# Kernel optimization log

Hardware: AMD Instinct MI355X
Metric: run time of the kernel (lower is better)

The kernel has to match this reference:

```python
import jax, jax.numpy as jnp
import numpy as np

T, D, H, E, K = 4096, 2048, 1408, 8, 2  # tokens, d_model, d_intermediate, n_experts, top_k


def setup_inputs() -> dict:
    key = jax.random.key(0)
    ks = jax.random.split(key, 5)
    x = jax.random.normal(ks[0], (T, D), dtype=jnp.float32)
    # distinct top-k expert ids per token (router output)
    indices = jnp.argsort(jax.random.uniform(ks[1], (T, E)), axis=-1)[:, :K].astype(jnp.int32)
    w = jax.random.uniform(ks[2], (T, K), dtype=jnp.float32) + 0.1
    weights = w / jnp.sum(w, axis=-1, keepdims=True)
    # stacked expert params: fc1 [E, 2H, D], fc2 [E, D, H] (nn.Linear layout)
    w1 = jax.random.normal(ks[3], (E, 2 * H, D), dtype=jnp.float32) * (D ** -0.5)
    w2 = jax.random.normal(ks[4], (E, D, H), dtype=jnp.float32) * (H ** -0.5)
    return {"x": x, "weights": weights, "indices": indices, "w1": w1, "w2": w2}


def reference(x, weights, indices, w1, w2):
    # combine weight per (expert, token): sum of routing weights where token routed to expert e
    onehot = jax.nn.one_hot(indices, E, dtype=x.dtype)          # [T, K, E]
    cw = jnp.einsum('tk,tke->et', weights, onehot)              # [E, T]

    def body(y, inp):
        w1_i, w2_i, cw_i = inp
        h = x @ w1_i.T                                          # [T, 2H]
        u, g = jnp.split(h, 2, axis=-1)                         # value, gate (chunk order of GatedMLP)
        out = (u * jax.nn.silu(g)) @ w2_i.T                     # [T, D]
        return y + out * cw_i[:, None], None

    y, _ = jax.lax.scan(body, jnp.zeros_like(x), (w1, w2, cw))
    return y
```

## Files before the change

### kernel.cpp

```cpp
#include <hip/hip_runtime.h>
#include <stdint.h>

#define T_TOK 4096
#define DMODEL 2048
#define HDIM 1408
#define NEXP 8
#define TOPK 2

#define BM 256
#define BN 256
#define BK 32
#define MAX_TILES (T_TOK * TOPK / BM + NEXP)
#define SMEM_BYTES (131072 + 1024)

typedef unsigned short u16;
typedef __bf16 bf16x8 __attribute__((ext_vector_type(8)));
typedef float f32x4 __attribute__((ext_vector_type(4)));

__device__ __forceinline__ u16 f2bf(float f) {
  union { float f; uint32_t u; } v; v.f = f;
  uint32_t r = (v.u + 0x7FFFu + ((v.u >> 16) & 1u)) >> 16;
  return (u16)r;
}

__device__ __forceinline__ void gll16(const void* g, void* l) {
  __builtin_amdgcn_global_load_lds(
      (__attribute__((address_space(1))) void*)(uintptr_t)g,
      (__attribute__((address_space(3))) void*)l, 16, 0, 0);
}

__global__ __launch_bounds__(256) void convert_all(
    const float* __restrict__ x, const float* __restrict__ w1,
    const float* __restrict__ w2, u16* __restrict__ xb,
    u16* __restrict__ w1b, u16* __restrict__ w2b) {
  const long c0 = (long)T_TOK * DMODEL / 8;
  const long c1 = (long)NEXP * 2 * HDIM * DMODEL / 8;
  const long c2 = (long)NEXP * DMODEL * HDIM / 8;
  const long total = c0 + c1 + c2;
  const long stride = (long)gridDim.x * blockDim.x;
  for (long i = blockIdx.x * (long)blockDim.x + threadIdx.x; i < total; i += stride) {
    const float* s; u16* d; long j;
    if (i < c0)            { s = x;  d = xb;  j = i; }
    else if (i < c0 + c1)  { s = w1; d = w1b; j = i - c0; }
    else                   { s = w2; d = w2b; j = i - c0 - c1; }
    const float4* sp = (const float4*)s + j * 2;
    float4 v0 = sp[0], v1 = sp[1];
    union { u16 us[8]; uint4 u4; } o;
    o.us[0] = f2bf(v0.x); o.us[1] = f2bf(v0.y); o.us[2] = f2bf(v0.z); o.us[3] = f2bf(v0.w);
    o.us[4] = f2bf(v1.x); o.us[5] = f2bf(v1.y); o.us[6] = f2bf(v1.z); o.us[7] = f2bf(v1.w);
    *((uint4*)(d + j * 8)) = o.u4;
  }
}

__global__ void route_kernel(const int* __restrict__ idx, int* __restrict__ cnt,
                             int* __restrict__ perm) {
  int i = blockIdx.x * blockDim.x + threadIdx.x;
  if (i < T_TOK * TOPK) {
    int e = idx[i];
    int p = atomicAdd(&cnt[e], 1);
    perm[e * T_TOK + p] = i;
  }
}

__global__ void tilemap_kernel(const int* __restrict__ cnt, int* __restrict__ tmap,
                               int* __restrict__ ntp) {
  if (threadIdx.x == 0 && blockIdx.x == 0) {
    int nt = 0;
    for (int e = 0; e < NEXP; ++e) {
      int n = cnt[e];
      for (int r = 0; r < n; r += BM) tmap[nt++] = (e << 16) | r;
    }
    *ntp = nt;
  }
}


template <int H, int VMN>
__device__ __forceinline__ void phase_core(const char* bc, const int (&aoffR)[8],
                                           const int (&boffR)[4], f32x4 (&acc)[8][4]) {
  bf16x8 a_[4], b_[4];
#pragma unroll
  for (int m = 0; m < 4; ++m) a_[m] = *(const bf16x8*)(bc + aoffR[H * 4 + m]);
#pragma unroll
  for (int n = 0; n < 4; ++n) b_[n] = *(const bf16x8*)(bc + boffR[n]);
  if constexpr (VMN == 8) {
    asm volatile("s_waitcnt vmcnt(8)" ::: "memory");
    __builtin_amdgcn_sched_barrier(0);
  } else if constexpr (VMN == 4) {
    asm volatile("s_waitcnt vmcnt(4)" ::: "memory");
    __builtin_amdgcn_sched_barrier(0);
  } else if constexpr (VMN == 0) {
    asm volatile("s_waitcnt vmcnt(0)" ::: "memory");
    __builtin_amdgcn_sched_barrier(0);
  }
  __builtin_amdgcn_s_barrier();
  __builtin_amdgcn_s_setprio(1);
#pragma unroll
  for (int m = 0; m < 4; ++m)
#pragma unroll
    for (int n = 0; n < 4; ++n)
      acc[H * 4 + m][n] = __builtin_amdgcn_mfma_f32_16x16x32_bf16(
          a_[m], b_[n], acc[H * 4 + m][n], 0, 0, 0);
  __builtin_amdgcn_s_setprio(0);
  __builtin_amdgcn_s_barrier();
}

template <int MODE>
__global__ __launch_bounds__(512, 2) void moe_gemm(
    const u16* __restrict__ A, const u16* __restrict__ Bw,
    const float* __restrict__ wts, const int* __restrict__ perm,
    const int* __restrict__ cnt, const int* __restrict__ tmap,
    const int* __restrict__ ntp, u16* __restrict__ act,
    float* __restrict__ pairs) {
  constexpr int KD = (MODE == 0) ? DMODEL : HDIM;
  constexpr int NT = KD / BK;
  extern __shared__ char smem[];
  int* rid_s = (int*)(smem + 131072);

  if ((int)blockIdx.x >= *ntp) return;
  const int tm = tmap[blockIdx.x];
  const int e = tm >> 16, r0 = tm & 0xFFFF;
  const int ne = cnt[e];
  const int tid = threadIdx.x;
  if (tid < BM) {
    int ii = r0 + tid;
    rid_s[tid] = perm[e * T_TOK + (ii < ne ? ii : ne - 1)];
  }
  __syncthreads();

  const int w = tid >> 6, l = tid & 63;
  const int wr = w >> 2, wc = w & 3;
  const int yb = blockIdx.y;

  const int ar1 = 32 * w + (l >> 2);
  const int ar2 = ar1 + 16;
  const int sslot = ((l & 3) ^ ((l >> 3) & 3)) * 8;
  long arow1, arow2;
  {
    int rid1 = rid_s[ar1], rid2 = rid_s[ar2];
    arow1 = (MODE == 0) ? (rid1 >> 1) : rid1;
    arow2 = (MODE == 0) ? (rid2 >> 1) : rid2;
  }
  const u16* aptr1 = A + arow1 * KD + sslot;
  const u16* aptr2 = A + arow2 * KD + sslot;
  long brow1, brow2;
  if constexpr (MODE == 0) {
    brow1 = (long)e * (2 * HDIM) + (ar1 < 128 ? yb * 128 + ar1 : HDIM + yb * 128 + ar1 - 128);
    brow2 = (long)e * (2 * HDIM) + (ar2 < 128 ? yb * 128 + ar2 : HDIM + yb * 128 + ar2 - 128);
  } else {
    brow1 = (long)e * DMODEL + yb * BN + ar1;
    brow2 = (long)e * DMODEL + yb * BN + ar2;
  }
  const u16* bptr1 = Bw + brow1 * KD + sslot;
  const u16* bptr2 = Bw + brow2 * KD + sslot;
  const int aoffL1 = 2 * w * 1024, aoffL2 = aoffL1 + 1024;
  const int boffL1 = 16384 + 2 * w * 1024, boffL2 = boffL1 + 1024;

  const int swz = ((l >> 4) ^ ((l >> 1) & 3)) * 16;
  int aoffR[8];
#pragma unroll
  for (int h = 0; h < 2; ++h)
#pragma unroll
    for (int m = 0; m < 4; ++m)
      aoffR[h * 4 + m] = (wr * 128 + h * 64 + m * 16 + (l & 15)) * 64 + swz;
  int boffR[4];
#pragma unroll
  for (int n = 0; n < 4; ++n)
    boffR[n] = 16384 + (wc * 64 + n * 16 + (l & 15)) * 64 + swz;

  f32x4 acc[8][4] = {};

#pragma unroll
  for (int tt = 0; tt < 3; ++tt) {
    char* sb = smem + tt * 32768;
    const size_t kq = (size_t)tt * BK;
    gll16(aptr1 + kq, sb + aoffL1);
    gll16(aptr2 + kq, sb + aoffL2);
    gll16(bptr1 + kq, sb + boffL1);
    gll16(bptr2 + kq, sb + boffL2);
  }
  asm volatile("s_waitcnt vmcnt(8)" ::: "memory");
  __builtin_amdgcn_sched_barrier(0);
  __builtin_amdgcn_s_barrier();

  for (int t = 0; t <= NT - 4; ++t) {
    const char* bufc = smem + (t & 3) * 32768;
    char* sb = smem + ((t + 3) & 3) * 32768;
    const size_t kq = (size_t)(t + 3) * BK;
    gll16(aptr1 + kq, sb + aoffL1);
    gll16(aptr2 + kq, sb + aoffL2);
    phase_core<0, -1>(bufc, aoffR, boffR, acc);
    gll16(bptr1 + kq, sb + boffL1);
    gll16(bptr2 + kq, sb + boffL2);
    phase_core<1, 8>(bufc, aoffR, boffR, acc);
  }
  {
    const char* bufc = smem + ((NT - 3) & 3) * 32768;
    phase_core<0, -1>(bufc, aoffR, boffR, acc);
    phase_core<1, 4>(bufc, aoffR, boffR, acc);
  }
  {
    const char* bufc = smem + ((NT - 2) & 3) * 32768;
    phase_core<0, -1>(bufc, aoffR, boffR, acc);
    phase_core<1, 0>(bufc, aoffR, boffR, acc);
  }
  {
    const char* bufc = smem + ((NT - 1) & 3) * 32768;
    phase_core<0, -1>(bufc, aoffR, boffR, acc);
    phase_core<1, -1>(bufc, aoffR, boffR, acc);
  }

  if constexpr (MODE == 0) {
    float* g_lds = (float*)smem;
    if (wc >= 2) {
      const int cl = (wc - 2) * 64;
#pragma unroll
      for (int mm = 0; mm < 8; ++mm)
#pragma unroll
        for (int n = 0; n < 4; ++n)
#pragma unroll
          for (int rg = 0; rg < 4; ++rg) {
            int row = wr * 128 + mm * 16 + (l >> 4) * 4 + rg;
            g_lds[row * 128 + cl + n * 16 + (l & 15)] = acc[mm][n][rg];
          }
    }
    __syncthreads();
    if (wc < 2) {
      const int cl = wc * 64;
#pragma unroll
      for (int mm = 0; mm < 8; ++mm) {
        const int rb = wr * 128 + mm * 16 + (l >> 4) * 4;
#pragma unroll
        for (int rg = 0; rg < 4; ++rg) {
          const int rloc = rb + rg;
          if (r0 + rloc >= ne) continue;
          const int rid = rid_s[rloc];
#pragma unroll
          for (int n = 0; n < 4; ++n) {
            const int col = cl + n * 16 + (l & 15);
            float g = g_lds[rloc * 128 + col];
            float u = acc[mm][n][rg];
            float val = u * (g / (1.f + __expf(-g)));
            act[(size_t)rid * HDIM + yb * 128 + col] = f2bf(val);
          }
        }
      }
    }
  } else {
#pragma unroll
    for (int mm = 0; mm < 8; ++mm) {
      const int rb = wr * 128 + mm * 16 + (l >> 4) * 4;
#pragma unroll
      for (int rg = 0; rg < 4; ++rg) {
        const int rloc = rb + rg;
        if (r0 + rloc >= ne) continue;
        const int rid = rid_s[rloc];
        const float wt = wts[rid];
#pragma unroll
        for (int n = 0; n < 4; ++n) {
          const int col = yb * BN + wc * 64 + n * 16 + (l & 15);
          pairs[(size_t)rid * DMODEL + col] = acc[mm][n][rg] * wt;
        }
      }
    }
  }
}

__global__ __launch_bounds__(256) void reduce_pairs(const float* __restrict__ pairs,
                                                    float* __restrict__ y) {
  const long total = (long)T_TOK * DMODEL / 4;
  const long stride = (long)gridDim.x * blockDim.x;
  for (long i = blockIdx.x * (long)blockDim.x + threadIdx.x; i < total; i += stride) {
    long t = (i * 4) / DMODEL;
    long d = (i * 4) % DMODEL;
    float4 a = *(const float4*)(pairs + (2 * t) * DMODEL + d);
    float4 b = *(const float4*)(pairs + (2 * t + 1) * DMODEL + d);
    float4 r;
    r.x = a.x + b.x; r.y = a.y + b.y; r.z = a.z + b.z; r.w = a.w + b.w;
    *(float4*)(y + t * DMODEL + d) = r;
  }
}

extern "C" void kernel_launch(void* const* d_in, const int* in_sizes, int n_in,
                              void* d_out, int out_size, void* d_ws, size_t ws_size,
                              hipStream_t stream) {
  const float* x = (const float*)d_in[0];
  const float* wts = (const float*)d_in[1];
  const int* idx = (const int*)d_in[2];
  const float* w1 = (const float*)d_in[3];
  const float* w2 = (const float*)d_in[4];
  float* y = (float*)d_out;

  char* ws = (char*)d_ws;
  size_t off = 0;
  int* cnt = (int*)(ws + off); off += 256;
  int* ntp = (int*)(ws + off); off += 256;
  int* tmap = (int*)(ws + off); off += 1024;
  int* perm = (int*)(ws + off); off += (size_t)NEXP * T_TOK * 4;
  off = (off + 255) & ~(size_t)255;
  size_t xb_off = off;
  u16* xb = (u16*)(ws + off);  off += (size_t)T_TOK * DMODEL * 2;
  u16* w1b = (u16*)(ws + off); off += (size_t)NEXP * 2 * HDIM * DMODEL * 2;
  u16* w2b = (u16*)(ws + off); off += (size_t)NEXP * DMODEL * HDIM * 2;
  u16* act = (u16*)(ws + off); off += (size_t)T_TOK * TOPK * HDIM * 2;
  float* pairs = (float*)(ws + xb_off);

  (void)hipFuncSetAttribute((const void*)moe_gemm<0>,
                            hipFuncAttributeMaxDynamicSharedMemorySize, SMEM_BYTES);
  (void)hipFuncSetAttribute((const void*)moe_gemm<1>,
                            hipFuncAttributeMaxDynamicSharedMemorySize, SMEM_BYTES);

  hipMemsetAsync(cnt, 0, 256, stream);
  convert_all<<<2048, 256, 0, stream>>>(x, w1, w2, xb, w1b, w2b);
  route_kernel<<<(T_TOK * TOPK + 255) / 256, 256, 0, stream>>>(idx, cnt, perm);
  tilemap_kernel<<<1, 64, 0, stream>>>(cnt, tmap, ntp);
  moe_gemm<0><<<dim3(MAX_TILES, HDIM / 128), 512, SMEM_BYTES, stream>>>(
      xb, w1b, wts, perm, cnt, tmap, ntp, act, nullptr);
  moe_gemm<1><<<dim3(MAX_TILES, DMODEL / BN), 512, SMEM_BYTES, stream>>>(
      act, w2b, wts, perm, cnt, tmap, ntp, nullptr, pairs);
  reduce_pairs<<<2048, 256, 0, stream>>>(pairs, y);
}
```

Baseline: 642.1 us.

## Restructure GEMM k-loop with one barrier per tile and in-register SwiGLU epilogue

The k-tile loop is rewritten so each step loads all 8 A fragments and 4 B fragments, issues the next tile's global-to-LDS loads, runs all 32 MFMAs, and then takes a single barrier. The old loop split each tile into two half-phases with two barriers each. The fc1 B-operand mapping is changed so every wave holds matching value and gate columns, which lets SiLU-gating happen in registers and drops the LDS round-trip and __syncthreads in the epilogue. The combined convert kernel is also split into three separate launches, removing the per-element branch at the cost of two extra launches. Keeping eight A fragments live raises register pressure, and fewer barriers means less latency hiding between the load waits.

```diff
diff --git a/kernel.cpp b/kernel.cpp
--- a/kernel.cpp
+++ b/kernel.cpp
@@ -29,26 +29,16 @@
       (__attribute__((address_space(3))) void*)l, 16, 0, 0);
 }
 
-__global__ __launch_bounds__(256) void convert_all(
-    const float* __restrict__ x, const float* __restrict__ w1,
-    const float* __restrict__ w2, u16* __restrict__ xb,
-    u16* __restrict__ w1b, u16* __restrict__ w2b) {
-  const long c0 = (long)T_TOK * DMODEL / 8;
-  const long c1 = (long)NEXP * 2 * HDIM * DMODEL / 8;
-  const long c2 = (long)NEXP * DMODEL * HDIM / 8;
-  const long total = c0 + c1 + c2;
+__global__ __launch_bounds__(256) void convert_k(const float* __restrict__ s,
+                                                 u16* __restrict__ d, long n8) {
   const long stride = (long)gridDim.x * blockDim.x;
-  for (long i = blockIdx.x * (long)blockDim.x + threadIdx.x; i < total; i += stride) {
-    const float* s; u16* d; long j;
-    if (i < c0)            { s = x;  d = xb;  j = i; }
-    else if (i < c0 + c1)  { s = w1; d = w1b; j = i - c0; }
-    else                   { s = w2; d = w2b; j = i - c0 - c1; }
-    const float4* sp = (const float4*)s + j * 2;
-    float4 v0 = sp[0], v1 = sp[1];
+  for (long i = blockIdx.x * (long)blockDim.x + threadIdx.x; i < n8; i += stride) {
+    float4 v0 = ((const float4*)s)[2 * i];
+    float4 v1 = ((const float4*)s)[2 * i + 1];
     union { u16 us[8]; uint4 u4; } o;
     o.us[0] = f2bf(v0.x); o.us[1] = f2bf(v0.y); o.us[2] = f2bf(v0.z); o.us[3] = f2bf(v0.w);
     o.us[4] = f2bf(v1.x); o.us[5] = f2bf(v1.y); o.us[6] = f2bf(v1.z); o.us[7] = f2bf(v1.w);
-    *((uint4*)(d + j * 8)) = o.u4;
+    ((uint4*)d)[i] = o.u4;
   }
 }
 
@@ -75,14 +65,30 @@
 }
 
 
-template <int H, int VMN>
-__device__ __forceinline__ void phase_core(const char* bc, const int (&aoffR)[8],
-                                           const int (&boffR)[4], f32x4 (&acc)[8][4]) {
-  bf16x8 a_[4], b_[4];
-#pragma unroll
-  for (int m = 0; m < 4; ++m) a_[m] = *(const bf16x8*)(bc + aoffR[H * 4 + m]);
+template <int VMN, bool STG, bool BAR>
+__device__ __forceinline__ void ktile(
+    const char* bc, char* sb, size_t kq,
+    const u16* aptr1, const u16* aptr2, const u16* bptr1, const u16* bptr2,
+    int aoffL1, int aoffL2, int boffL1, int boffL2,
+    const int (&aoffR)[8], const int (&boffR)[4], f32x4 (&acc)[8][4]) {
+  bf16x8 a_[8], b_[4];
+#pragma unroll
+  for (int m = 0; m < 8; ++m) a_[m] = *(const bf16x8*)(bc + aoffR[m]);
 #pragma unroll
   for (int n = 0; n < 4; ++n) b_[n] = *(const bf16x8*)(bc + boffR[n]);
+  if constexpr (STG) {
+    gll16(aptr1 + kq, sb + aoffL1);
+    gll16(aptr2 + kq, sb + aoffL2);
+    gll16(bptr1 + kq, sb + boffL1);
+    gll16(bptr2 + kq, sb + boffL2);
+  }
+  __builtin_amdgcn_s_setprio(1);
+#pragma unroll
+  for (int m = 0; m < 8; ++m)
+#pragma unroll
+    for (int n = 0; n < 4; ++n)
+      acc[m][n] = __builtin_amdgcn_mfma_f32_16x16x32_bf16(a_[m], b_[n], acc[m][n], 0, 0, 0);
+  __builtin_amdgcn_s_setprio(0);
   if constexpr (VMN == 8) {
     asm volatile("s_waitcnt vmcnt(8)" ::: "memory");
     __builtin_amdgcn_sched_barrier(0);
@@ -93,16 +99,7 @@
     asm volatile("s_waitcnt vmcnt(0)" ::: "memory");
     __builtin_amdgcn_sched_barrier(0);
   }
-  __builtin_amdgcn_s_barrier();
-  __builtin_amdgcn_s_setprio(1);
-#pragma unroll
-  for (int m = 0; m < 4; ++m)
-#pragma unroll
-    for (int n = 0; n < 4; ++n)
-      acc[H * 4 + m][n] = __builtin_amdgcn_mfma_f32_16x16x32_bf16(
-          a_[m], b_[n], acc[H * 4 + m][n], 0, 0, 0);
-  __builtin_amdgcn_s_setprio(0);
-  __builtin_amdgcn_s_barrier();
+  if constexpr (BAR) __builtin_amdgcn_s_barrier();
 }
 
 template <int MODE>
@@ -159,14 +156,18 @@
   const int swz = ((l >> 4) ^ ((l >> 1) & 3)) * 16;
   int aoffR[8];
 #pragma unroll
-  for (int h = 0; h < 2; ++h)
-#pragma unroll
-    for (int m = 0; m < 4; ++m)
-      aoffR[h * 4 + m] = (wr * 128 + h * 64 + m * 16 + (l & 15)) * 64 + swz;
+  for (int m = 0; m < 8; ++m)
+    aoffR[m] = (wr * 128 + m * 16 + (l & 15)) * 64 + swz;
   int boffR[4];
 #pragma unroll
-  for (int n = 0; n < 4; ++n)
-    boffR[n] = 16384 + (wc * 64 + n * 16 + (l & 15)) * 64 + swz;
+  for (int n = 0; n < 4; ++n) {
+    int br;
+    if constexpr (MODE == 0)
+      br = (n < 2) ? (wc * 32 + n * 16 + (l & 15)) : (128 + wc * 32 + (n - 2) * 16 + (l & 15));
+    else
+      br = wc * 64 + n * 16 + (l & 15);
+    boffR[n] = 16384 + br * 64 + swz;
+  }
 
   f32x4 acc[8][4] = {};
 
@@ -183,66 +184,36 @@
   __builtin_amdgcn_sched_barrier(0);
   __builtin_amdgcn_s_barrier();
 
-  for (int t = 0; t <= NT - 4; ++t) {
-    const char* bufc = smem + (t & 3) * 32768;
-    char* sb = smem + ((t + 3) & 3) * 32768;
-    const size_t kq = (size_t)(t + 3) * BK;
-    gll16(aptr1 + kq, sb + aoffL1);
-    gll16(aptr2 + kq, sb + aoffL2);
-    phase_core<0, -1>(bufc, aoffR, boffR, acc);
-    gll16(bptr1 + kq, sb + boffL1);
-    gll16(bptr2 + kq, sb + boffL2);
-    phase_core<1, 8>(bufc, aoffR, boffR, acc);
-  }
-  {
-    const char* bufc = smem + ((NT - 3) & 3) * 32768;
-    phase_core<0, -1>(bufc, aoffR, boffR, acc);
-    phase_core<1, 4>(bufc, aoffR, boffR, acc);
-  }
-  {
-    const char* bufc = smem + ((NT - 2) & 3) * 32768;
-    phase_core<0, -1>(bufc, aoffR, boffR, acc);
-    phase_core<1, 0>(bufc, aoffR, boffR, acc);
-  }
-  {
-    const char* bufc = smem + ((NT - 1) & 3) * 32768;
-    phase_core<0, -1>(bufc, aoffR, boffR, acc);
-    phase_core<1, -1>(bufc, aoffR, boffR, acc);
-  }
+  for (int t = 0; t <= NT - 4; ++t)
+    ktile<8, true, true>(smem + (t & 3) * 32768, smem + ((t + 3) & 3) * 32768,
+                         (size_t)(t + 3) * BK, aptr1, aptr2, bptr1, bptr2,
+                         aoffL1, aoffL2, boffL1, boffL2, aoffR, boffR, acc);
+  ktile<4, false, true>(smem + ((NT - 3) & 3) * 32768, nullptr, 0,
+                        aptr1, aptr2, bptr1, bptr2,
+                        aoffL1, aoffL2, boffL1, boffL2, aoffR, boffR, acc);
+  ktile<0, false, true>(smem + ((NT - 2) & 3) * 32768, nullptr, 0,
+                        aptr1, aptr2, bptr1, bptr2,
+                        aoffL1, aoffL2, boffL1, boffL2, aoffR, boffR, acc);
+  ktile<-1, false, false>(smem + ((NT - 1) & 3) * 32768, nullptr, 0,
+                          aptr1, aptr2, bptr1, bptr2,
+                          aoffL1, aoffL2, boffL1, boffL2, aoffR, boffR, acc);
 
   if constexpr (MODE == 0) {
-    float* g_lds = (float*)smem;
-    if (wc >= 2) {
-      const int cl = (wc - 2) * 64;
-#pragma unroll
-      for (int mm = 0; mm < 8; ++mm)
-#pragma unroll
-        for (int n = 0; n < 4; ++n)
-#pragma unroll
-          for (int rg = 0; rg < 4; ++rg) {
-            int row = wr * 128 + mm * 16 + (l >> 4) * 4 + rg;
-            g_lds[row * 128 + cl + n * 16 + (l & 15)] = acc[mm][n][rg];
-          }
-    }
-    __syncthreads();
-    if (wc < 2) {
-      const int cl = wc * 64;
-#pragma unroll
-      for (int mm = 0; mm < 8; ++mm) {
-        const int rb = wr * 128 + mm * 16 + (l >> 4) * 4;
-#pragma unroll
-        for (int rg = 0; rg < 4; ++rg) {
-          const int rloc = rb + rg;
-          if (r0 + rloc >= ne) continue;
-          const int rid = rid_s[rloc];
-#pragma unroll
-          for (int n = 0; n < 4; ++n) {
-            const int col = cl + n * 16 + (l & 15);
-            float g = g_lds[rloc * 128 + col];
-            float u = acc[mm][n][rg];
-            float val = u * (g / (1.f + __expf(-g)));
-            act[(size_t)rid * HDIM + yb * 128 + col] = f2bf(val);
-          }
+#pragma unroll
+    for (int mm = 0; mm < 8; ++mm) {
+      const int rb = wr * 128 + mm * 16 + (l >> 4) * 4;
+#pragma unroll
+      for (int rg = 0; rg < 4; ++rg) {
+        const int rloc = rb + rg;
+        if (r0 + rloc >= ne) continue;
+        const int rid = rid_s[rloc];
+#pragma unroll
+        for (int n = 0; n < 2; ++n) {
+          const int col = yb * 128 + wc * 32 + n * 16 + (l & 15);
+          float u = acc[mm][n][rg];
+          float g = acc[mm][n + 2][rg];
+          float val = u * (g / (1.f + __expf(-g)));
+          act[(size_t)rid * HDIM + col] = f2bf(val);
         }
       }
     }
@@ -311,7 +282,9 @@
                             hipFuncAttributeMaxDynamicSharedMemorySize, SMEM_BYTES);
 
   hipMemsetAsync(cnt, 0, 256, stream);
-  convert_all<<<2048, 256, 0, stream>>>(x, w1, w2, xb, w1b, w2b);
+  convert_k<<<2048, 256, 0, stream>>>(x, xb, (long)T_TOK * DMODEL / 8);
+  convert_k<<<2048, 256, 0, stream>>>(w1, w1b, (long)NEXP * 2 * HDIM * DMODEL / 8);
+  convert_k<<<2048, 256, 0, stream>>>(w2, w2b, (long)NEXP * DMODEL * HDIM / 8);
   route_kernel<<<(T_TOK * TOPK + 255) / 256, 256, 0, stream>>>(idx, cnt, perm);
   tilemap_kernel<<<1, 64, 0, stream>>>(cnt, tmap, ntp);
   moe_gemm<0><<<dim3(MAX_TILES, HDIM / 128), 512, SMEM_BYTES, stream>>>(
```

Measured after the change: 617.7 us. 1.04x faster.
